# Kernel tuning notes

Measured on AMD Instinct MI355X. Metric: run time of the kernel, lower is better.

Reference implementation:

```python
import jax, jax.numpy as jnp
import numpy as np

EPS = 1e-12  # torch F.normalize eps

def setup_inputs() -> dict:
    key = jax.random.key(0)
    ks = jax.random.split(key, 3)
    B, N, C, H, K = 4, 4096, 512, 8, 64
    x = jax.random.normal(ks[0], (B, N, C), dtype=jnp.float32)
    W_qkvv = jax.random.normal(ks[1], (4 * C, C), dtype=jnp.float32) * (1.0 / np.sqrt(C))
    # init_: uniform(-1/sqrt(K), 1/sqrt(K)) over [N, K]
    std = 1.0 / np.sqrt(K)
    EF = jax.random.uniform(ks[2], (N, K), dtype=jnp.float32, minval=-std, maxval=std)
    temperature = jnp.ones((H, 1, 1), dtype=jnp.float32)
    temperature2 = jnp.ones((H, 1, 1), dtype=jnp.float32)
    return {"x": x, "W_qkvv": W_qkvv, "EF": EF,
            "temperature": temperature, "temperature2": temperature2}

def _l2norm(t):
    # torch.nn.functional.normalize(dim=-1): x / max(||x||_2, eps)
    n = jnp.sqrt(jnp.sum(t * t, axis=-1, keepdims=True))
    return t / jnp.maximum(n, EPS)

def reference(x, W_qkvv, EF, temperature, temperature2):
    B, N, C = x.shape
    H = temperature.shape[0]
    d = C // H
    # fused QKVV projection (no bias)
    qkvv = (x @ W_qkvv.T).reshape(B, N, 4, H, d)
    qkvv = jnp.transpose(qkvv, (2, 0, 3, 1, 4))  # [4,B,H,N,d]
    # transpose last two dims -> [B,H,d,N]
    q = jnp.swapaxes(qkvv[0], -2, -1)
    k = jnp.swapaxes(qkvv[1], -2, -1)
    v_CA = jnp.swapaxes(qkvv[2], -2, -1)
    v_SA = jnp.swapaxes(qkvv[3], -2, -1)
    # Linformer-style EF projection over token axis: [B,H,d,N] x [N,K] -> [B,H,d,K]
    k_proj = jnp.einsum('bhdn,nk->bhdk', k, EF)
    v_proj = jnp.einsum('bhdn,nk->bhdk', v_SA, EF)
    # L2-normalize q,k over token axis
    qn = _l2norm(q)
    kn = _l2norm(k)
    # channel attention: [B,H,d,d]
    attn_CA = jax.nn.softmax(jnp.einsum('bhdn,bhen->bhde', qn, kn) * temperature, axis=-1)
    x_CA = jnp.einsum('bhde,bhen->bhdn', attn_CA, v_CA)           # [B,H,d,N]
    x_CA = jnp.transpose(x_CA, (0, 3, 1, 2)).reshape(B, N, C)      # [B,N,C]
    # spatial attention via projected K: [B,H,N,K]
    attn_SA = jax.nn.softmax(jnp.einsum('bhdn,bhdk->bhnk', qn, k_proj) * temperature2, axis=-1)
    x_SA = jnp.einsum('bhnk,bhdk->bhnd', attn_SA, v_proj)          # [B,H,N,d]
    # faithful to the original: permute(0,3,1,2) then reshape(B,N,C)
    x_SA = jnp.transpose(x_SA, (0, 3, 1, 2)).reshape(B, N, C)
    return x_CA + x_SA
```

## Files before the change

kernel.cpp:

```cpp
#include <hip/hip_runtime.h>

typedef unsigned short u16;
typedef unsigned int u32;
typedef __attribute__((ext_vector_type(8))) short s16x8;
typedef __attribute__((ext_vector_type(4))) float f32x4;

#define MFMA16(a,b,c) __builtin_amdgcn_mfma_f32_16x16x32_bf16(a,b,c,0,0,0)

__device__ __forceinline__ u16 f2bf(float f){
  u32 u = __builtin_bit_cast(u32, f);
  return (u16)((u + 0x7FFFu + ((u >> 16) & 1u)) >> 16);
}
__device__ __forceinline__ float b2f(u16 s){
  u32 u = ((u32)s) << 16;
  return __builtin_bit_cast(float, u);
}
__device__ __forceinline__ void async16(const void* g, void* l){
  __builtin_amdgcn_global_load_lds((const __attribute__((address_space(1))) u32*)g,
                                   (__attribute__((address_space(3))) u32*)l, 16, 0, 0);
}


__global__ __launch_bounds__(256) void k_convert(const float4* __restrict__ x4,
                                                 const float4* __restrict__ w4,
                                                 const float* __restrict__ EF,
                                                 u16* __restrict__ Xb, u16* __restrict__ Wb,
                                                 u16* __restrict__ EFt){
  int i = blockIdx.x * 256 + threadIdx.x;
  if (i < 2097152){
    float4 v = x4[i];
    u32 lo = (u32)f2bf(v.x) | ((u32)f2bf(v.y) << 16);
    u32 hi = (u32)f2bf(v.z) | ((u32)f2bf(v.w) << 16);
    *(uint2*)(&Xb[(size_t)i*4]) = make_uint2(lo, hi);
  } else if (i < 2097152 + 262144){
    int j = i - 2097152;
    float4 v = w4[j];
    u32 lo = (u32)f2bf(v.x) | ((u32)f2bf(v.y) << 16);
    u32 hi = (u32)f2bf(v.z) | ((u32)f2bf(v.w) << 16);
    *(uint2*)(&Wb[(size_t)j*4]) = make_uint2(lo, hi);
  } else if (i < 2097152 + 262144 + 262144){
    int j = i - 2097152 - 262144;
    int kk = j >> 12, nn = j & 4095;
    EFt[(size_t)kk*4096 + nn] = f2bf(EF[(size_t)nn*64 + kk]);
  }
}

__global__ __launch_bounds__(256) void k_gemm(const u16* __restrict__ Wb,
                                              const u16* __restrict__ Xb,
                                              u16* __restrict__ Out){
  __shared__ u16 smA[128*32];
  __shared__ u16 smB[128*32];
  int bid = blockIdx.x;
  int sbid = (bid & 7) * 256 + (bid >> 3);
  int ot = sbid & 15, mt = sbid >> 4;
  int o0 = ot * 128, m0 = mt * 128;
  int t = threadIdx.x;
  int lane = t & 63, w = t >> 6;
  int wr = w >> 1, wc = w & 1;
  int l15 = lane & 15, l4 = lane >> 4;
  f32x4 acc[4][4];
#pragma unroll
  for (int a = 0; a < 4; ++a)
#pragma unroll
    for (int b = 0; b < 4; ++b) acc[a][b] = (f32x4){0.f, 0.f, 0.f, 0.f};

  for (int kt = 0; kt < 16; ++kt){
    int kb = kt * 32;
#pragma unroll
    for (int i = 0; i < 2; ++i){
      int la = t + 256 * i;
      int row = la >> 2, sl = la & 3;
      int sg = sl ^ ((row >> 1) & 3);
      async16(Wb + (size_t)(o0 + row) * 512 + kb + sg * 8, &smA[la * 8]);
      async16(Xb + (size_t)(m0 + row) * 512 + kb + sg * 8, &smB[la * 8]);
    }
    __syncthreads();
    s16x8 af[4], bfr[4];
#pragma unroll
    for (int rf = 0; rf < 4; ++rf){
      int row = wr*64 + rf*16 + l15;
      af[rf] = *(const s16x8*)(&smA[row*32 + ((l4 ^ ((row >> 1) & 3)))*8]);
    }
#pragma unroll
    for (int cf = 0; cf < 4; ++cf){
      int row = wc*64 + cf*16 + l15;
      bfr[cf] = *(const s16x8*)(&smB[row*32 + ((l4 ^ ((row >> 1) & 3)))*8]);
    }
#pragma unroll
    for (int rf = 0; rf < 4; ++rf)
#pragma unroll
      for (int cf = 0; cf < 4; ++cf)
        acc[rf][cf] = MFMA16(af[rf], bfr[cf], acc[rf][cf]);
    __syncthreads();
  }
#pragma unroll
  for (int rf = 0; rf < 4; ++rf)
#pragma unroll
    for (int cf = 0; cf < 4; ++cf){
      int o = o0 + wr*64 + rf*16 + l4*4;
      int m = m0 + wc*64 + cf*16 + l15;
#pragma unroll
      for (int r = 0; r < 4; ++r) Out[(size_t)(o + r) * 16384 + m] = f2bf(acc[rf][cf][r]);
    }
}

__global__ __launch_bounds__(256) void k_rnorm(const u16* __restrict__ QK,
                                               float* __restrict__ rq, float* __restrict__ rk){
  int job = blockIdx.x * 4 + (threadIdx.x >> 6);
  int o = job >> 2, b = job & 3;
  int lane = threadIdx.x & 63;
  const u16* row = QK + (size_t)o * 16384 + (size_t)b * 4096;
  float s = 0.f;
#pragma unroll
  for (int it = 0; it < 8; ++it){
    s16x8 v = *(const s16x8*)(&row[it * 512 + lane * 8]);
#pragma unroll
    for (int j = 0; j < 8; ++j){ float f = b2f((u16)v[j]); s += f * f; }
  }
  for (int off = 32; off; off >>= 1) s += __shfl_down(s, off);
  if (lane == 0){
    float r = 1.f / fmaxf(sqrtf(s), 1e-12f);
    if (o < 512) rq[b * 512 + o] = r;
    else         rk[b * 512 + (o - 512)] = r;
  }
}

__global__ __launch_bounds__(256) void k_acc1(const u16* __restrict__ QK,
                                              const u16* __restrict__ EFt,
                                              float* __restrict__ Pp){
  __shared__ u16 Ab[2][64*128];
  __shared__ u16 Bb[2][64*128];
  int bid = blockIdx.x;
  int p = bid >> 8;
  int rem = bid & 255;
  int bh = rem >> 3, s = rem & 7;
  int b = bh >> 3, h = bh & 7;
  int t = threadIdx.x, lane = t & 63, w = t >> 6, l15 = lane & 15, l4 = lane >> 4;
  int abase = (p == 0 ? 0 : (p == 1 ? 512 : 1536)) + h * 64;
  const u16* Aglob = QK + (size_t)abase * 16384 + (size_t)b * 4096 + s * 512;
  const u16* Bglob;
  size_t bstride;
  if (p == 0){ Bglob = QK + (size_t)(512 + h*64) * 16384 + (size_t)b * 4096 + s * 512; bstride = 16384; }
  else       { Bglob = EFt + s * 512; bstride = 4096; }
  int srow = t >> 4, sslot = t & 15;

#define STAGE_ACC(ch, buf)                                                        \
  {                                                                               \
    int n0_ = (ch) * 128;                                                         \
    _Pragma("unroll")                                                             \
    for (int c = 0; c < 4; ++c){                                                  \
      int row = c*16 + srow;                                                      \
      int sg = sslot ^ (row & 7);                                                 \
      async16(Aglob + (size_t)row * 16384 + n0_ + sg*8, &Ab[buf][row*128 + sslot*8]); \
    }                                                                             \
    _Pragma("unroll")                                                             \
    for (int c = 0; c < 4; ++c){                                                  \
      int row = c*16 + srow;                                                      \
      int sg = sslot ^ (row & 7);                                                 \
      async16(Bglob + (size_t)row * bstride + n0_ + sg*8, &Bb[buf][row*128 + sslot*8]); \
    }                                                                             \
  }

  f32x4 acc[4];
#pragma unroll
  for (int c = 0; c < 4; ++c) acc[c] = (f32x4){0.f,0.f,0.f,0.f};

  STAGE_ACC(0, 0);
#pragma unroll
  for (int ch = 0; ch < 4; ++ch){
    int buf = ch & 1;
    if (ch < 3){
      STAGE_ACC(ch + 1, buf ^ 1);
      asm volatile("s_waitcnt vmcnt(8)" ::: "memory");
    } else {
      asm volatile("s_waitcnt vmcnt(0)" ::: "memory");
    }
    __builtin_amdgcn_s_barrier();
    asm volatile("" ::: "memory");
    int arow = w*16 + l15;
#pragma unroll
    for (int ks = 0; ks < 4; ++ks){
      s16x8 a = *(const s16x8*)(&Ab[buf][arow*128 + (((ks*4 + l4) ^ (arow & 7)))*8]);
#pragma unroll
      for (int cf = 0; cf < 4; ++cf){
        int brow = cf*16 + l15;
        s16x8 bb = *(const s16x8*)(&Bb[buf][brow*128 + (((ks*4 + l4) ^ (brow & 7)))*8]);
        acc[cf] = MFMA16(a, bb, acc[cf]);
      }
    }
    __builtin_amdgcn_s_barrier();
    asm volatile("" ::: "memory");
  }

  float* out = Pp + ((size_t)(bh * 3 + p) * 8 + s) * 4096;
#pragma unroll
  for (int cf = 0; cf < 4; ++cf)
#pragma unroll
    for (int r = 0; r < 4; ++r){
      int rr = w*16 + l4*4 + r;
      int cc = cf*16 + l15;
      int off = (p == 1) ? (cc * 64 + rr) : (rr * 64 + cc);
      out[off] = acc[cf][r];
    }
#undef STAGE_ACC
}

__global__ __launch_bounds__(256) void k_fin(const float* __restrict__ Pp,
                                             const float* __restrict__ rq,
                                             const float* __restrict__ rk,
                                             const float* __restrict__ t1,
                                             const float* __restrict__ t2,
                                             u16* __restrict__ Pca,
                                             u16* __restrict__ kpb,
                                             u16* __restrict__ vpb){
  int bh = blockIdx.x;
  int b = bh >> 3, h = bh & 7;
  int t = threadIdx.x;
  int row = t >> 2, q4 = t & 3;
  const float* base = Pp + (size_t)bh * 3 * 8 * 4096;
  float t1h = t1[h], t2h = t2[h];
  const float* rqh = rq + b*512 + h*64;
  const float* rkh = rk + b*512 + h*64;
  int sA = (((q4*2)     ^ (row & 7)) << 3);
  int sB = (((q4*2 + 1) ^ (row & 7)) << 3);

  {
    float v[16];
#pragma unroll
    for (int i = 0; i < 4; ++i){
      f32x4 a = (f32x4){0.f,0.f,0.f,0.f};
#pragma unroll
      for (int s = 0; s < 8; ++s)
        a += *(const f32x4*)(base + (size_t)s * 4096 + t*16 + i*4);
#pragma unroll
      for (int j = 0; j < 4; ++j) v[i*4 + j] = a[j];
    }
    float sq = rqh[row] * t1h;
#pragma unroll
    for (int e = 0; e < 16; ++e) v[e] *= sq * rkh[q4*16 + e];
    float mx = v[0];
#pragma unroll
    for (int e = 1; e < 16; ++e) mx = fmaxf(mx, v[e]);
    mx = fmaxf(mx, __shfl_xor(mx, 1));
    mx = fmaxf(mx, __shfl_xor(mx, 2));
    float sum = 0.f;
#pragma unroll
    for (int e = 0; e < 16; ++e){ v[e] = __expf(v[e] - mx); sum += v[e]; }
    sum += __shfl_xor(sum, 1);
    sum += __shfl_xor(sum, 2);
    float inv = 1.f / sum;
    s16x8 o0, o1;
#pragma unroll
    for (int e = 0; e < 8; ++e){ o0[e] = (short)f2bf(v[e] * inv); o1[e] = (short)f2bf(v[8+e] * inv); }
    *(s16x8*)(&Pca[(size_t)bh*4096 + row*64 + sA]) = o0;
    *(s16x8*)(&Pca[(size_t)bh*4096 + row*64 + sB]) = o1;
  }
  {
    const float* p1 = base + 8 * 4096;
    float v[16];
#pragma unroll
    for (int i = 0; i < 4; ++i){
      f32x4 a = (f32x4){0.f,0.f,0.f,0.f};
#pragma unroll
      for (int s = 0; s < 8; ++s)
        a += *(const f32x4*)(p1 + (size_t)s * 4096 + t*16 + i*4);
#pragma unroll
      for (int j = 0; j < 4; ++j) v[i*4 + j] = a[j];
    }
    s16x8 o0, o1;
#pragma unroll
    for (int e = 0; e < 8; ++e){
      o0[e] = (short)f2bf(v[e]   * rqh[q4*16 + e]     * t2h);
      o1[e] = (short)f2bf(v[8+e] * rqh[q4*16 + 8 + e] * t2h);
    }
    *(s16x8*)(&kpb[(size_t)bh*4096 + row*64 + sA]) = o0;
    *(s16x8*)(&kpb[(size_t)bh*4096 + row*64 + sB]) = o1;
  }
  {
    const float* p2 = base + 16 * 4096;
    float v[16];
#pragma unroll
    for (int i = 0; i < 4; ++i){
      f32x4 a = (f32x4){0.f,0.f,0.f,0.f};
#pragma unroll
      for (int s = 0; s < 8; ++s)
        a += *(const f32x4*)(p2 + (size_t)s * 4096 + t*16 + i*4);
#pragma unroll
      for (int j = 0; j < 4; ++j) v[i*4 + j] = a[j];
    }
    s16x8 o0, o1;
#pragma unroll
    for (int e = 0; e < 8; ++e){ o0[e] = (short)f2bf(v[e]); o1[e] = (short)f2bf(v[8+e]); }
    *(s16x8*)(&vpb[(size_t)bh*4096 + row*64 + sA]) = o0;
    *(s16x8*)(&vpb[(size_t)bh*4096 + row*64 + sB]) = o1;
  }
}

__global__ __launch_bounds__(256) void k_ca_pv(const u16* __restrict__ QK,
                                               const u16* __restrict__ Pca,
                                               float* __restrict__ out){
  __shared__ u16 Pl[64*64];
  __shared__ u16 Vt[64*64];
  __shared__ float Sx[64*64];
  int bid = blockIdx.x;
  int ch = bid & 63, bh = bid >> 6, b = bh >> 3, h = bh & 7;
  int n0 = ch * 64;
  int t = threadIdx.x, lane = t & 63, w = t >> 6, l15 = lane & 15, l4 = lane >> 4;
  {
    const u16* src = Pca + (size_t)bh * 4096;
#pragma unroll
    for (int c = 0; c < 2; ++c)
      async16(src + (c*256 + t)*8, &Pl[(c*256 + t)*8]);
  }
  const u16* Vg = QK + (size_t)(1024 + h*64) * 16384 + (size_t)b*4096 + n0;
#pragma unroll
  for (int pass = 0; pass < 2; ++pass){
    int idx = pass*256 + t;
    int e = idx >> 3, j0 = (idx & 7) * 8;
    s16x8 v = *(const s16x8*)(Vg + (size_t)e * 16384 + j0);
#pragma unroll
    for (int i = 0; i < 8; ++i){
      int j = j0 + i;
      Vt[j*64 + ((((e>>3) ^ (j & 7))) << 3) + (e & 7)] = (u16)v[i];
    }
  }
  __syncthreads();
  f32x4 acc[4];
#pragma unroll
  for (int c = 0; c < 4; ++c) acc[c] = (f32x4){0.f,0.f,0.f,0.f};
  int ar = w*16 + l15;
#pragma unroll
  for (int ks = 0; ks < 2; ++ks){
    s16x8 a = *(const s16x8*)(&Pl[ar*64 + (((ks*4 + l4) ^ (ar & 7)))*8]);
#pragma unroll
    for (int cf = 0; cf < 4; ++cf){
      int br = cf*16 + l15;
      s16x8 bb = *(const s16x8*)(&Vt[br*64 + (((ks*4 + l4) ^ (br & 7)))*8]);
      acc[cf] = MFMA16(a, bb, acc[cf]);
    }
  }
#pragma unroll
  for (int cf = 0; cf < 4; ++cf)
#pragma unroll
    for (int r = 0; r < 4; ++r){
      int d = w*16 + l4*4 + r, j = cf*16 + l15;
      Sx[j*64 + d] = acc[cf][r];
    }
  __syncthreads();
#pragma unroll
  for (int i = 0; i < 4; ++i){
    int idx = t + 256 * i;
    int j = idx >> 4, v = idx & 15;
    float4 val;
    val.x = Sx[j*64 + v*4 + 0]; val.y = Sx[j*64 + v*4 + 1];
    val.z = Sx[j*64 + v*4 + 2]; val.w = Sx[j*64 + v*4 + 3];
    *(float4*)(&out[((size_t)(b*4096 + n0 + j)) * 512 + h*64 + v*4]) = val;
  }
}

__global__ __launch_bounds__(256) void k_sa(const u16* __restrict__ QK,
                                            const u16* __restrict__ kpb,
                                            const u16* __restrict__ vpb,
                                            float* __restrict__ out){
  __shared__ u16 Qt[64*64];
  __shared__ u16 kpl[64*64];
  __shared__ u16 vpl[64*64];
  __shared__ float Sf[64*64];
  int bid = blockIdx.x;
  int ch = bid & 63, bh = bid >> 6, b = bh >> 3, h = bh & 7;
  int n0 = ch * 64;
  int t = threadIdx.x, lane = t & 63, w = t >> 6, l15 = lane & 15, l4 = lane >> 4;
#pragma unroll
  for (int c = 0; c < 2; ++c){
    async16(kpb + (size_t)bh*4096 + (c*256 + t)*8, &kpl[(c*256 + t)*8]);
    async16(vpb + (size_t)bh*4096 + (c*256 + t)*8, &vpl[(c*256 + t)*8]);
  }
  const u16* Qg = QK + (size_t)(h*64) * 16384 + (size_t)b*4096 + n0;
#pragma unroll
  for (int pass = 0; pass < 2; ++pass){
    int idx = pass*256 + t;
    int dd = idx >> 3, j0 = (idx & 7) * 8;
    s16x8 v = *(const s16x8*)(Qg + (size_t)dd * 16384 + j0);
#pragma unroll
    for (int i = 0; i < 8; ++i){
      int j = j0 + i;
      Qt[j*64 + ((((dd>>3) ^ (j & 7))) << 3) + (dd & 7)] = (u16)v[i];
    }
  }
  __syncthreads();
  f32x4 acc[4];
#pragma unroll
  for (int c = 0; c < 4; ++c) acc[c] = (f32x4){0.f,0.f,0.f,0.f};
  int ar = w*16 + l15;
#pragma unroll
  for (int ks = 0; ks < 2; ++ks){
    s16x8 a = *(const s16x8*)(&Qt[ar*64 + (((ks*4 + l4) ^ (ar & 7)))*8]);
#pragma unroll
    for (int cf = 0; cf < 4; ++cf){
      int br = cf*16 + l15;
      s16x8 bb = *(const s16x8*)(&kpl[br*64 + (((ks*4 + l4) ^ (br & 7)))*8]);
      acc[cf] = MFMA16(a, bb, acc[cf]);
    }
  }
#pragma unroll
  for (int r = 0; r < 4; ++r){
    float mx = fmaxf(fmaxf(acc[0][r], acc[1][r]), fmaxf(acc[2][r], acc[3][r]));
    mx = fmaxf(mx, __shfl_xor(mx, 1));
    mx = fmaxf(mx, __shfl_xor(mx, 2));
    mx = fmaxf(mx, __shfl_xor(mx, 4));
    mx = fmaxf(mx, __shfl_xor(mx, 8));
    float sum = 0.f;
#pragma unroll
    for (int cf = 0; cf < 4; ++cf){ acc[cf][r] = __expf(acc[cf][r] - mx); sum += acc[cf][r]; }
    sum += __shfl_xor(sum, 1);
    sum += __shfl_xor(sum, 2);
    sum += __shfl_xor(sum, 4);
    sum += __shfl_xor(sum, 8);
    float inv = 1.f / sum;
#pragma unroll
    for (int cf = 0; cf < 4; ++cf) acc[cf][r] *= inv;
  }
#pragma unroll
  for (int cf = 0; cf < 4; ++cf)
#pragma unroll
    for (int r = 0; r < 4; ++r){
      int j = w*16 + l4*4 + r;
      int kslot = cf*2 + (l15 >> 3);
      Qt[j*64 + ((kslot ^ (j & 7)) << 3) + (l15 & 7)] = f2bf(acc[cf][r]);
    }
  __syncthreads();
  f32x4 acc2[4];
#pragma unroll
  for (int c = 0; c < 4; ++c) acc2[c] = (f32x4){0.f,0.f,0.f,0.f};
#pragma unroll
  for (int ks = 0; ks < 2; ++ks){
    s16x8 a = *(const s16x8*)(&Qt[ar*64 + (((ks*4 + l4) ^ (ar & 7)))*8]);
#pragma unroll
    for (int cf = 0; cf < 4; ++cf){
      int br = cf*16 + l15;
      s16x8 bb = *(const s16x8*)(&vpl[br*64 + (((ks*4 + l4) ^ (br & 7)))*8]);
      acc2[cf] = MFMA16(a, bb, acc2[cf]);
    }
  }
#pragma unroll
  for (int cf = 0; cf < 4; ++cf)
#pragma unroll
    for (int r = 0; r < 4; ++r){
      int j = w*16 + l4*4 + r, dd = cf*16 + l15;
      Sf[dd*64 + j] = acc2[cf][r];
    }
  __syncthreads();
#pragma unroll
  for (int i = 0; i < 4; ++i){
    int idx = t + 256 * i;
    int dd = idx >> 4, v = idx & 15;
    size_t p = (size_t)b*2097152 + (size_t)dd*32768 + (size_t)h*4096 + n0 + v*4;
    float4 cur = *(float4*)(&out[p]);
    cur.x += Sf[dd*64 + v*4 + 0]; cur.y += Sf[dd*64 + v*4 + 1];
    cur.z += Sf[dd*64 + v*4 + 2]; cur.w += Sf[dd*64 + v*4 + 3];
    *(float4*)(&out[p]) = cur;
  }
}

extern "C" void kernel_launch(void* const* d_in, const int* in_sizes, int n_in,
                              void* d_out, int out_size, void* d_ws, size_t ws_size,
                              hipStream_t stream) {
  const float* x  = (const float*)d_in[0];
  const float* Wq = (const float*)d_in[1];
  const float* EF = (const float*)d_in[2];
  const float* t1 = (const float*)d_in[3];
  const float* t2 = (const float*)d_in[4];
  float* out = (float*)d_out;

  u16* Xb  = (u16*)d_ws;
  u16* Wb  = Xb + 8388608;
  u16* EFt = Wb + 1048576;
  u16* QK  = EFt + 262144;
  float* rq  = (float*)(QK + 33554432);
  float* rk  = rq + 2048;
  u16* kpb = (u16*)(rk + 2048);
  u16* vpb = kpb + 131072;
  u16* Pca = vpb + 131072;
  float* Pp = (float*)d_ws;

  k_convert<<<10240, 256, 0, stream>>>((const float4*)x, (const float4*)Wq, EF, Xb, Wb, EFt);
  k_gemm   <<<2048, 256, 0, stream>>>(Wb, Xb, QK);
  k_rnorm  <<<1024, 256, 0, stream>>>(QK, rq, rk);
  k_acc1   <<<768,  256, 0, stream>>>(QK, EFt, Pp);
  k_fin    <<<32,   256, 0, stream>>>(Pp, rq, rk, t1, t2, Pca, kpb, vpb);
  k_ca_pv  <<<2048, 256, 0, stream>>>(QK, Pca, out);
  k_sa     <<<2048, 256, 0, stream>>>(QK, kpb, vpb, out);
}
```

Baseline: 198.6 us.

## Rewrite projection GEMM as 256x256 double-buffered 8-wave tile; stagger transpose LDS writes

The QKVV projection GEMM moves from 128x128 tiles with a single LDS buffer and K-step 32 to 256x256 tiles with 512 threads, K-step 64, and a double-buffered async global-to-LDS prefetch of the next K tile. Raw barriers and s_setprio bracket the MFMA bursts so loads overlap compute. The aim is more operand reuse per byte loaded and hidden load latency, at the cost of 128KB of LDS and more accumulator registers per thread. Separately, the transpose stores into LDS in the CA-PV and SA kernels now rotate their element order per thread to cut LDS bank conflicts.

```diff
diff --git a/kernel.cpp b/kernel.cpp
--- a/kernel.cpp
+++ b/kernel.cpp
@@ -45,59 +45,91 @@
   }
 }
 
-__global__ __launch_bounds__(256) void k_gemm(const u16* __restrict__ Wb,
-                                              const u16* __restrict__ Xb,
-                                              u16* __restrict__ Out){
-  __shared__ u16 smA[128*32];
-  __shared__ u16 smB[128*32];
+__global__ __launch_bounds__(512, 2) void k_gemm(const u16* __restrict__ Wb,
+                                                 const u16* __restrict__ Xb,
+                                                 u16* __restrict__ Out){
+  __shared__ u16 As[2][2][128*64];
+  __shared__ u16 Bs[2][2][128*64];
   int bid = blockIdx.x;
-  int sbid = (bid & 7) * 256 + (bid >> 3);
-  int ot = sbid & 15, mt = sbid >> 4;
-  int o0 = ot * 128, m0 = mt * 128;
+  int sbid = (bid & 7) * 64 + (bid >> 3);
+  int ot = sbid >> 6, mt = sbid & 63;
+  int o0 = ot * 256, m0 = mt * 256;
   int t = threadIdx.x;
-  int lane = t & 63, w = t >> 6;
-  int wr = w >> 1, wc = w & 1;
+  int lane = t & 63, wid = t >> 6;
+  int wr = wid >> 2, wc = wid & 3;
   int l15 = lane & 15, l4 = lane >> 4;
-  f32x4 acc[4][4];
-#pragma unroll
-  for (int a = 0; a < 4; ++a)
+
+#define STAGE_TILE(kt_, db_)                                                    \
+  {                                                                             \
+    int kb_ = (kt_) * 64;                                                       \
+    int srow_ = t >> 3, sg_ = (t & 7) ^ (srow_ & 7);                            \
+    _Pragma("unroll")                                                           \
+    for (int hf = 0; hf < 2; ++hf){                                             \
+      _Pragma("unroll")                                                         \
+      for (int c = 0; c < 2; ++c){                                              \
+        int row = c*64 + srow_;                                                 \
+        async16(Wb + (size_t)(o0 + hf*128 + row) * 512 + kb_ + sg_*8,           \
+                &As[db_][hf][row*64 + (t & 7)*8]);                              \
+        async16(Xb + (size_t)(m0 + hf*128 + row) * 512 + kb_ + sg_*8,           \
+                &Bs[db_][hf][row*64 + (t & 7)*8]);                              \
+      }                                                                         \
+    }                                                                           \
+  }
+
+  f32x4 acc[8][4];
+#pragma unroll
+  for (int a = 0; a < 8; ++a)
 #pragma unroll
     for (int b = 0; b < 4; ++b) acc[a][b] = (f32x4){0.f, 0.f, 0.f, 0.f};
 
-  for (int kt = 0; kt < 16; ++kt){
-    int kb = kt * 32;
-#pragma unroll
-    for (int i = 0; i < 2; ++i){
-      int la = t + 256 * i;
-      int row = la >> 2, sl = la & 3;
-      int sg = sl ^ ((row >> 1) & 3);
-      async16(Wb + (size_t)(o0 + row) * 512 + kb + sg * 8, &smA[la * 8]);
-      async16(Xb + (size_t)(m0 + row) * 512 + kb + sg * 8, &smB[la * 8]);
-    }
-    __syncthreads();
-    s16x8 af[4], bfr[4];
-#pragma unroll
-    for (int rf = 0; rf < 4; ++rf){
-      int row = wr*64 + rf*16 + l15;
-      af[rf] = *(const s16x8*)(&smA[row*32 + ((l4 ^ ((row >> 1) & 3)))*8]);
-    }
+  STAGE_TILE(0, 0);
+  asm volatile("s_waitcnt vmcnt(0)" ::: "memory");
+  __builtin_amdgcn_s_barrier();
+  asm volatile("" ::: "memory");
+
+  s16x8 bfr[4];
+  for (int kt = 0; kt < 8; ++kt){
+    int db = kt & 1;
+    const u16* Abase = &As[db][wr][0];
+    const u16* Bbase = &Bs[db][wc >> 1][0];
+#pragma unroll
+    for (int p = 0; p < 4; ++p){
+      const int ks = p >> 1, rfh = p & 1;
+      s16x8 af[4];
+#pragma unroll
+      for (int i = 0; i < 4; ++i){
+        int row = (rfh*4 + i)*16 + l15;
+        af[i] = *(const s16x8*)(Abase + row*64 + ((ks*4 + l4) ^ (row & 7))*8);
+      }
+      if (rfh == 0){
+#pragma unroll
+        for (int cf = 0; cf < 4; ++cf){
+          int row = (wc & 1)*64 + cf*16 + l15;
+          bfr[cf] = *(const s16x8*)(Bbase + row*64 + ((ks*4 + l4) ^ (row & 7))*8);
+        }
+      }
+      if (p == 0 && kt < 7) STAGE_TILE(kt + 1, db ^ 1);
+      __builtin_amdgcn_s_barrier();
+      asm volatile("" ::: "memory");
+      __builtin_amdgcn_s_setprio(1);
+#pragma unroll
+      for (int i = 0; i < 4; ++i)
+#pragma unroll
+        for (int cf = 0; cf < 4; ++cf)
+          acc[rfh*4 + i][cf] = MFMA16(af[i], bfr[cf], acc[rfh*4 + i][cf]);
+      __builtin_amdgcn_s_setprio(0);
+      if (p == 3 && kt < 7) asm volatile("s_waitcnt vmcnt(0)" ::: "memory");
+      __builtin_amdgcn_s_barrier();
+      asm volatile("" ::: "memory");
+    }
+  }
+#undef STAGE_TILE
+
+#pragma unroll
+  for (int rf = 0; rf < 8; ++rf)
 #pragma unroll
     for (int cf = 0; cf < 4; ++cf){
-      int row = wc*64 + cf*16 + l15;
-      bfr[cf] = *(const s16x8*)(&smB[row*32 + ((l4 ^ ((row >> 1) & 3)))*8]);
-    }
-#pragma unroll
-    for (int rf = 0; rf < 4; ++rf)
-#pragma unroll
-      for (int cf = 0; cf < 4; ++cf)
-        acc[rf][cf] = MFMA16(af[rf], bfr[cf], acc[rf][cf]);
-    __syncthreads();
-  }
-#pragma unroll
-  for (int rf = 0; rf < 4; ++rf)
-#pragma unroll
-    for (int cf = 0; cf < 4; ++cf){
-      int o = o0 + wr*64 + rf*16 + l4*4;
+      int o = o0 + wr*128 + rf*16 + l4*4;
       int m = m0 + wc*64 + cf*16 + l15;
 #pragma unroll
       for (int r = 0; r < 4; ++r) Out[(size_t)(o + r) * 16384 + m] = f2bf(acc[rf][cf][r]);
@@ -316,12 +348,13 @@
 #pragma unroll
   for (int pass = 0; pass < 2; ++pass){
     int idx = pass*256 + t;
-    int e = idx >> 3, j0 = (idx & 7) * 8;
+    int e = idx >> 3, j0 = (idx & 7) * 8, g = idx & 7;
     s16x8 v = *(const s16x8*)(Vg + (size_t)e * 16384 + j0);
 #pragma unroll
     for (int i = 0; i < 8; ++i){
-      int j = j0 + i;
-      Vt[j*64 + ((((e>>3) ^ (j & 7))) << 3) + (e & 7)] = (u16)v[i];
+      int jj = (i + e + g) & 7;
+      int j = j0 + jj;
+      Vt[j*64 + ((((e>>3) ^ jj)) << 3) + (e & 7)] = (u16)v[jj];
     }
   }
   __syncthreads();
@@ -379,12 +412,13 @@
 #pragma unroll
   for (int pass = 0; pass < 2; ++pass){
     int idx = pass*256 + t;
-    int dd = idx >> 3, j0 = (idx & 7) * 8;
+    int dd = idx >> 3, j0 = (idx & 7) * 8, g = idx & 7;
     s16x8 v = *(const s16x8*)(Qg + (size_t)dd * 16384 + j0);
 #pragma unroll
     for (int i = 0; i < 8; ++i){
-      int j = j0 + i;
-      Qt[j*64 + ((((dd>>3) ^ (j & 7))) << 3) + (dd & 7)] = (u16)v[i];
+      int jj = (i + dd + g) & 7;
+      int j = j0 + jj;
+      Qt[j*64 + ((((dd>>3) ^ jj)) << 3) + (dd & 7)] = (u16)v[jj];
     }
   }
   __syncthreads();
@@ -484,7 +518,7 @@
   float* Pp = (float*)d_ws;
 
   k_convert<<<10240, 256, 0, stream>>>((const float4*)x, (const float4*)Wq, EF, Xb, Wb, EFt);
-  k_gemm   <<<2048, 256, 0, stream>>>(Wb, Xb, QK);
+  k_gemm   <<<512,  512, 0, stream>>>(Wb, Xb, QK);
   k_rnorm  <<<1024, 256, 0, stream>>>(QK, rq, rk);
   k_acc1   <<<768,  256, 0, stream>>>(QK, EFt, Pp);
   k_fin    <<<32,   256, 0, stream>>>(Pp, rq, rk, t1, t2, Pca, kpb, vpb);
```

After: 198.7 us. Within noise of the previous version (+0.0%).
